# Kernel optimization log

Hardware: AMD Instinct MI355X
Metric: run time of the kernel (lower is better)

The kernel has to match this reference:

```python
import jax, jax.numpy as jnp
import numpy as np

NUM_HEADS = 16
D_MODEL = 1024


def setup_inputs() -> dict:
    key = jax.random.key(0)
    k1, k2 = jax.random.split(key)
    x = jax.random.normal(k1, (4, 2048, D_MODEL), dtype=jnp.float32)
    # kqv Linear(d_model, 3*d_model, bias=False); stored as [in, out] for x @ W
    W_kqv = jax.random.normal(k2, (D_MODEL, 3 * D_MODEL), dtype=jnp.float32) * (D_MODEL ** -0.5)
    return {"x": x, "W_kqv": W_kqv}


def _alibi_slopes(num_heads):
    # 1 / ((2**8)**((i+1)/num_heads)) for each head
    base = (2.0 ** 8) ** (1.0 / num_heads)
    return jnp.asarray([1.0 / base ** (i + 1) for i in range(num_heads)], dtype=jnp.float32)


def reference(x, W_kqv):
    B, S, D = x.shape
    H = NUM_HEADS
    hd = D // H
    scale = jnp.sqrt(jnp.float32(D))  # note: sqrt(d_model), faithful to source

    kqv = x @ W_kqv  # [B, S, 3D]; chunk order in source: key, query, value
    k, q, v = jnp.split(kqv, 3, axis=-1)
    # [B, H, S, hd]
    q = q.reshape(B, S, H, hd).transpose(0, 2, 1, 3)
    k = k.reshape(B, S, H, hd).transpose(0, 2, 1, 3)
    v = v.reshape(B, S, H, hd).transpose(0, 2, 1, 3)

    # ALiBi bias: m[h] * (j - i), shape [1, H, S, S]
    pos = jnp.arange(S)
    rel = (pos[None, :] - pos[:, None]).astype(jnp.float32)  # [S, S]
    m = _alibi_slopes(H)  # [H]
    bias = m[:, None, None] * rel  # [H, S, S]

    score = jnp.einsum('bhsd,bhnd->bhsn', q, k) / scale + bias[None]
    attn = jax.nn.softmax(score, axis=-1)
    out = jnp.einsum('bhsn,bhnd->bhsd', attn, v)  # [B, H, S, hd]
    out = out.transpose(0, 2, 1, 3).reshape(B, S, D)
    return out
```

## Files before the change

kernel.cpp:

```cpp
#include <hip/hip_runtime.h>
#include <stdint.h>

typedef __bf16 bf16;
typedef __bf16 bf16x4 __attribute__((ext_vector_type(4)));
typedef __bf16 bf16x8 __attribute__((ext_vector_type(8)));
typedef float f32x4 __attribute__((ext_vector_type(4)));

#define AS1 __attribute__((address_space(1)))
#define AS3 __attribute__((address_space(3)))


__global__ void cvt_x_kernel(const float* __restrict__ x, bf16* __restrict__ xb) {
    int i = blockIdx.x * 256 + threadIdx.x;
    const float4* x4 = (const float4*)x;
    float4 a = x4[i * 2];
    float4 b = x4[i * 2 + 1];
    bf16x8 o;
    o[0] = (bf16)a.x; o[1] = (bf16)a.y; o[2] = (bf16)a.z; o[3] = (bf16)a.w;
    o[4] = (bf16)b.x; o[5] = (bf16)b.y; o[6] = (bf16)b.z; o[7] = (bf16)b.w;
    *(bf16x8*)(xb + (size_t)i * 8) = o;
}

__global__ void cvt_w_kernel(const float* __restrict__ w, bf16* __restrict__ wt) {
    __shared__ float tile[32][33];
    int nt = blockIdx.x, kt = blockIdx.y;
    int tx = threadIdx.x, ty = threadIdx.y;
#pragma unroll
    for (int j = 0; j < 4; ++j)
        tile[ty + j * 8][tx] = w[(size_t)(kt * 32 + ty + j * 8) * 3072 + nt * 32 + tx];
    __syncthreads();
#pragma unroll
    for (int j = 0; j < 4; ++j)
        wt[(size_t)(nt * 32 + ty + j * 8) * 1024 + kt * 32 + tx] = (bf16)tile[tx][ty + j * 8];
}

__global__ __launch_bounds__(256) void gemm_kqv_kernel(
    const bf16* __restrict__ xb, const bf16* __restrict__ wt,
    bf16* __restrict__ kb, bf16* __restrict__ qb, bf16* __restrict__ vt) {
    __shared__ bf16 As[2][128 * 32];
    __shared__ bf16 Bs[2][128 * 32];
    int bid = blockIdx.x;
    int bm = bid / 24, bn = bid % 24;
    int m0 = bm * 128, n0 = bn * 128;
    int t = threadIdx.x;
    int lane = t & 63, wid = t >> 6;
    int g = lane >> 4, l15 = lane & 15;
    int wr = wid >> 1, wc = wid & 1;

    f32x4 acc[4][4] = {};

    auto stageAB = [&](int ks, int buf) {
        int k0 = ks * 32;
#pragma unroll
        for (int c = 0; c < 2; ++c) {
            int slot = c * 256 + t;
            int row = slot >> 2, kk = (slot & 3) * 8;
            __builtin_amdgcn_global_load_lds(
                (const AS1 void*)(xb + (size_t)(m0 + row) * 1024 + k0 + kk),
                (AS3 void*)(&As[buf][slot * 8]), 16, 0, 0);
        }
#pragma unroll
        for (int c = 0; c < 2; ++c) {
            int slot = c * 256 + t;
            int row = slot >> 2, kk = (slot & 3) * 8;
            __builtin_amdgcn_global_load_lds(
                (const AS1 void*)(wt + (size_t)(n0 + row) * 1024 + k0 + kk),
                (AS3 void*)(&Bs[buf][slot * 8]), 16, 0, 0);
        }
    };

    stageAB(0, 0);
    for (int ks = 0; ks < 32; ++ks) {
        __syncthreads();
        if (ks + 1 < 32) stageAB(ks + 1, (ks + 1) & 1);
        const bf16* Ab = As[ks & 1];
        const bf16* Bb = Bs[ks & 1];
        bf16x8 af[4], bfr[4];
#pragma unroll
        for (int mi = 0; mi < 4; ++mi)
            af[mi] = *(const bf16x8*)(Ab + (wr * 64 + mi * 16 + l15) * 32 + g * 8);
#pragma unroll
        for (int ni = 0; ni < 4; ++ni)
            bfr[ni] = *(const bf16x8*)(Bb + (wc * 64 + ni * 16 + l15) * 32 + g * 8);
#pragma unroll
        for (int mi = 0; mi < 4; ++mi)
#pragma unroll
            for (int ni = 0; ni < 4; ++ni)
                acc[mi][ni] = __builtin_amdgcn_mfma_f32_16x16x32_bf16(
                    af[mi], bfr[ni], acc[mi][ni], 0, 0, 0);
    }

    int tsel = n0 >> 10;
#pragma unroll
    for (int mi = 0; mi < 4; ++mi) {
#pragma unroll
        for (int ni = 0; ni < 4; ++ni) {
#pragma unroll
            for (int r = 0; r < 4; ++r) {
                int row = m0 + wr * 64 + mi * 16 + g * 4 + r;
                int col = n0 + wc * 64 + ni * 16 + l15;
                int b = row >> 11, s = row & 2047;
                int cc = col & 1023;
                int h = cc >> 6, d = cc & 63;
                int bh = b * 16 + h;
                float v = acc[mi][ni][r];
                if (tsel == 0)      kb[((size_t)bh * 2048 + s) * 64 + d] = (bf16)v;
                else if (tsel == 1) qb[((size_t)bh * 2048 + s) * 64 + d] = (bf16)(v * 0.0450842503f);
                else                vt[((size_t)bh * 64 + d) * 2048 + s] = (bf16)v;
            }
        }
    }
}

__global__ __launch_bounds__(256) void attn_kernel(
    const bf16* __restrict__ qb, const bf16* __restrict__ kb,
    const bf16* __restrict__ vt, float* __restrict__ out) {
    __shared__ bf16 Kl[64 * 64];
    __shared__ bf16 Vl[2][64 * 64];
    __shared__ bf16 Pl[4][32 * 64];
    int bid = blockIdx.x;
    int bh = bid >> 4, qt = bid & 15;
    int b = bh >> 4, h = bh & 15;
    int t = threadIdx.x, lane = t & 63, wid = t >> 6;
    int g = lane >> 4, l15 = lane & 15;
    int q0 = qt * 128 + wid * 32;
    float mh2 = exp2f(-0.5f * (float)(h + 1)) * 1.44269504f;

    const bf16* Qp = qb + ((size_t)bh * 2048 + q0) * 64;
    const bf16* Kp = kb + (size_t)bh * 2048 * 64;
    const bf16* Vp = vt + (size_t)bh * 64 * 2048;

    bf16x8 qf[2][2];
#pragma unroll
    for (int qi = 0; qi < 2; ++qi)
#pragma unroll
        for (int kk = 0; kk < 2; ++kk)
            qf[qi][kk] = *(const bf16x8*)(Qp + (size_t)(qi * 16 + l15) * 64 + kk * 32 + g * 8);

    f32x4 oacc[2][4] = {};
    float mrun[2], lrun[2];
    mrun[0] = mrun[1] = -3.0e38f;
    lrun[0] = lrun[1] = 0.f;

    float jb[4], rb[4];
#pragma unroll
    for (int ji = 0; ji < 4; ++ji) jb[ji] = mh2 * (float)(ji * 16 + g * 4);
#pragma unroll
    for (int r = 0; r < 4; ++r) rb[r] = mh2 * (float)r;

    auto stageK = [&](int tile) {
        int j0 = tile * 64;
#pragma unroll
        for (int c = 0; c < 2; ++c) {
            int slot = c * 256 + t;
            int row = slot >> 3;
            int cs = (slot & 7) ^ (row & 7);
            __builtin_amdgcn_global_load_lds(
                (const AS1 void*)(Kp + (size_t)(j0 + row) * 64 + cs * 8),
                (AS3 void*)(&Kl[slot * 8]), 16, 0, 0);
        }
    };
    auto stageV = [&](int tile, int buf) {
        int j0 = tile * 64;
#pragma unroll
        for (int c = 0; c < 2; ++c) {
            int slot = c * 256 + t;
            int row = slot >> 3;
            int cs = (slot & 7) ^ (row & 7);
            __builtin_amdgcn_global_load_lds(
                (const AS1 void*)(Vp + (size_t)row * 2048 + j0 + cs * 8),
                (AS3 void*)(&Vl[buf][slot * 8]), 16, 0, 0);
        }
    };

    stageK(0);
    stageV(0, 0);
    bf16* Pw = Pl[wid];

    for (int tile = 0; tile < 32; ++tile) {
        __syncthreads();
        const bf16* Vb = Vl[tile & 1];

        float tb = mh2 * (float)(tile * 64);
        f32x4 sc[2][4];
#pragma unroll
        for (int ji = 0; ji < 4; ++ji) {
            float base = tb + jb[ji];
#pragma unroll
            for (int r = 0; r < 4; ++r) {
                float v = base + rb[r];
                sc[0][ji][r] = v;
                sc[1][ji][r] = v;
            }
        }
#pragma unroll
        for (int ji = 0; ji < 4; ++ji) {
#pragma unroll
            for (int kk = 0; kk < 2; ++kk) {
                int row = ji * 16 + l15;
                int c16 = (kk * 4 + g) ^ (row & 7);
                bf16x8 kf = *(const bf16x8*)(Kl + row * 64 + c16 * 8);
#pragma unroll
                for (int qi = 0; qi < 2; ++qi)
                    sc[qi][ji] = __builtin_amdgcn_mfma_f32_16x16x32_bf16(
                        kf, qf[qi][kk], sc[qi][ji], 0, 0, 0);
            }
        }
        __syncthreads();
        if (tile + 1 < 32) {
            stageK(tile + 1);
            stageV(tile + 1, (tile + 1) & 1);
        }

        float pmx[2];
#pragma unroll
        for (int qi = 0; qi < 2; ++qi) {
            float m0a = fmaxf(fmaxf(sc[qi][0][0], sc[qi][0][1]), fmaxf(sc[qi][0][2], sc[qi][0][3]));
            float m1a = fmaxf(fmaxf(sc[qi][1][0], sc[qi][1][1]), fmaxf(sc[qi][1][2], sc[qi][1][3]));
            float m2a = fmaxf(fmaxf(sc[qi][2][0], sc[qi][2][1]), fmaxf(sc[qi][2][2], sc[qi][2][3]));
            float m3a = fmaxf(fmaxf(sc[qi][3][0], sc[qi][3][1]), fmaxf(sc[qi][3][2], sc[qi][3][3]));
            pmx[qi] = fmaxf(fmaxf(m0a, m1a), fmaxf(m2a, m3a));
        }

        int stable = (pmx[0] <= mrun[0] + 8.0f && pmx[1] <= mrun[1] + 8.0f) ? 1 : 0;
        if (!__all(stable)) {
            float corr[2];
#pragma unroll
            for (int qi = 0; qi < 2; ++qi) {
                float mx = pmx[qi];
                mx = fmaxf(mx, __shfl_xor(mx, 16));
                mx = fmaxf(mx, __shfl_xor(mx, 32));
                float mnew = fmaxf(mrun[qi], mx);
                corr[qi] = __builtin_amdgcn_exp2f(mrun[qi] - mnew);
                mrun[qi] = mnew;
                lrun[qi] *= corr[qi];
            }
#pragma unroll
            for (int qi = 0; qi < 2; ++qi)
#pragma unroll
                for (int r = 0; r < 4; ++r) {
                    float cB = __shfl(corr[qi], g * 4 + r);
#pragma unroll
                    for (int di = 0; di < 4; ++di) oacc[qi][di][r] *= cB;
                }
        }

#pragma unroll
        for (int qi = 0; qi < 2; ++qi) {
            float mq = mrun[qi];
            float s = 0.f;
#pragma unroll
            for (int ji = 0; ji < 4; ++ji)
#pragma unroll
                for (int r = 0; r < 4; ++r) {
                    float p = __builtin_amdgcn_exp2f(sc[qi][ji][r] - mq);
                    sc[qi][ji][r] = p;
                    s += p;
                }
            s += __shfl_xor(s, 16);
            s += __shfl_xor(s, 32);
            lrun[qi] += s;
        }

#pragma unroll
        for (int qi = 0; qi < 2; ++qi) {
            int qloc = qi * 16 + l15;
            int base = qloc * 64;
            int swz = (qloc & 7) * 8;
#pragma unroll
            for (int ji = 0; ji < 4; ++ji) {
                bf16x4 pv;
                pv[0] = (bf16)sc[qi][ji][0];
                pv[1] = (bf16)sc[qi][ji][1];
                pv[2] = (bf16)sc[qi][ji][2];
                pv[3] = (bf16)sc[qi][ji][3];
                *(bf16x4*)(Pw + base + ((ji * 16 + g * 4) ^ swz)) = pv;
            }
        }

#pragma unroll
        for (int kk = 0; kk < 2; ++kk) {
            bf16x8 pf[2];
#pragma unroll
            for (int qi = 0; qi < 2; ++qi) {
                int qloc = qi * 16 + l15;
                pf[qi] = *(const bf16x8*)(Pw + qloc * 64 + ((kk * 32 + g * 8) ^ ((qloc & 7) * 8)));
            }
#pragma unroll
            for (int di = 0; di < 4; ++di) {
                int row = di * 16 + l15;
                int c16 = (kk * 4 + g) ^ (row & 7);
                bf16x8 vf = *(const bf16x8*)(Vb + row * 64 + c16 * 8);
#pragma unroll
                for (int qi = 0; qi < 2; ++qi)
                    oacc[qi][di] = __builtin_amdgcn_mfma_f32_16x16x32_bf16(
                        pf[qi], vf, oacc[qi][di], 0, 0, 0);
            }
        }
    }

#pragma unroll
    for (int qi = 0; qi < 2; ++qi) {
#pragma unroll
        for (int r = 0; r < 4; ++r) {
            float lq = __shfl(lrun[qi], g * 4 + r);
            float inv = 1.0f / lq;
            int s = q0 + qi * 16 + g * 4 + r;
            float* op = out + ((size_t)b * 2048 + s) * 1024 + h * 64;
#pragma unroll
            for (int di = 0; di < 4; ++di)
                op[di * 16 + l15] = oacc[qi][di][r] * inv;
        }
    }
}

extern "C" void kernel_launch(void* const* d_in, const int* in_sizes, int n_in,
                              void* d_out, int out_size, void* d_ws, size_t ws_size,
                              hipStream_t stream) {
    (void)in_sizes; (void)n_in; (void)out_size; (void)ws_size;
    const float* x = (const float*)d_in[0];
    const float* w = (const float*)d_in[1];
    float* out = (float*)d_out;
    char* ws = (char*)d_ws;
    bf16* xb = (bf16*)(ws);
    bf16* wt = (bf16*)(ws + 16777216);
    bf16* kb = (bf16*)(ws + 23068672);
    bf16* qb = (bf16*)(ws + 39845888);
    bf16* vt = (bf16*)(ws + 56623104);

    cvt_x_kernel<<<4096, 256, 0, stream>>>(x, xb);
    cvt_w_kernel<<<dim3(96, 32), dim3(32, 8), 0, stream>>>(w, wt);
    gemm_kqv_kernel<<<1536, 256, 0, stream>>>(xb, wt, kb, qb, vt);
    attn_kernel<<<1024, 256, 0, stream>>>(qb, kb, vt, out);
}
```

Measured before the change: 311.7 us.

## Fold running max into score init, use 3-input max, vectorize V-transpose stores

The attention kernel now subtracts the running max when it seeds the MFMA accumulator with the ALiBi bias. This removes the per-element subtraction before exp2 in the common path, and the max reduction is regrouped into three-input fmax calls. The initial running max changes from -3e38 to -10000 to avoid overflow in the folded form, which assumes scores never fall that low. The QKV projection epilogue is restructured with hoisted index math and bf16x4 vector stores for the transposed V output.

```diff
diff --git a/kernel.cpp b/kernel.cpp
--- a/kernel.cpp
+++ b/kernel.cpp
@@ -9,6 +9,10 @@
 #define AS1 __attribute__((address_space(1)))
 #define AS3 __attribute__((address_space(3)))
 
+
+__device__ __forceinline__ float f3(float a, float b, float c) {
+    return fmaxf(fmaxf(a, b), c);
+}
 
 __global__ void cvt_x_kernel(const float* __restrict__ x, bf16* __restrict__ xb) {
     int i = blockIdx.x * 256 + threadIdx.x;
@@ -91,24 +95,39 @@
     }
 
     int tsel = n0 >> 10;
-#pragma unroll
-    for (int mi = 0; mi < 4; ++mi) {
+    int hbase = (n0 >> 6) & 15;
+    int bidx = m0 >> 11;
+    int m0b = (m0 & 2047) + wr * 64 + g * 4;
+    int bh = bidx * 16 + hbase + wc;
+    if (tsel == 2) {
 #pragma unroll
         for (int ni = 0; ni < 4; ++ni) {
-#pragma unroll
-            for (int r = 0; r < 4; ++r) {
-                int row = m0 + wr * 64 + mi * 16 + g * 4 + r;
-                int col = n0 + wc * 64 + ni * 16 + l15;
-                int b = row >> 11, s = row & 2047;
-                int cc = col & 1023;
-                int h = cc >> 6, d = cc & 63;
-                int bh = b * 16 + h;
-                float v = acc[mi][ni][r];
-                if (tsel == 0)      kb[((size_t)bh * 2048 + s) * 64 + d] = (bf16)v;
-                else if (tsel == 1) qb[((size_t)bh * 2048 + s) * 64 + d] = (bf16)(v * 0.0450842503f);
-                else                vt[((size_t)bh * 64 + d) * 2048 + s] = (bf16)v;
-            }
-        }
+            int d = ni * 16 + l15;
+            bf16* vbase = vt + ((size_t)bh * 64 + d) * 2048 + m0b;
+#pragma unroll
+            for (int mi = 0; mi < 4; ++mi) {
+                bf16x4 pv;
+                pv[0] = (bf16)acc[mi][ni][0];
+                pv[1] = (bf16)acc[mi][ni][1];
+                pv[2] = (bf16)acc[mi][ni][2];
+                pv[3] = (bf16)acc[mi][ni][3];
+                *(bf16x4*)(vbase + mi * 16) = pv;
+            }
+        }
+    } else {
+        bf16* dst = (tsel == 0) ? kb : qb;
+        float sc = (tsel == 0) ? 1.0f : 0.0450842503f;
+#pragma unroll
+        for (int mi = 0; mi < 4; ++mi)
+#pragma unroll
+            for (int ni = 0; ni < 4; ++ni) {
+                int d = ni * 16 + l15;
+#pragma unroll
+                for (int r = 0; r < 4; ++r) {
+                    int s = m0b + mi * 16 + r;
+                    dst[((size_t)bh * 2048 + s) * 64 + d] = (bf16)(acc[mi][ni][r] * sc);
+                }
+            }
     }
 }
 
@@ -139,7 +158,7 @@
 
     f32x4 oacc[2][4] = {};
     float mrun[2], lrun[2];
-    mrun[0] = mrun[1] = -3.0e38f;
+    mrun[0] = mrun[1] = -10000.0f;
     lrun[0] = lrun[1] = 0.f;
 
     float jb[4], rb[4];
@@ -184,13 +203,13 @@
         float tb = mh2 * (float)(tile * 64);
         f32x4 sc[2][4];
 #pragma unroll
-        for (int ji = 0; ji < 4; ++ji) {
-            float base = tb + jb[ji];
-#pragma unroll
-            for (int r = 0; r < 4; ++r) {
-                float v = base + rb[r];
-                sc[0][ji][r] = v;
-                sc[1][ji][r] = v;
+        for (int qi = 0; qi < 2; ++qi) {
+            float bq = tb - mrun[qi];
+#pragma unroll
+            for (int ji = 0; ji < 4; ++ji) {
+                float base = bq + jb[ji];
+#pragma unroll
+                for (int r = 0; r < 4; ++r) sc[qi][ji][r] = base + rb[r];
             }
         }
 #pragma unroll
@@ -215,26 +234,35 @@
         float pmx[2];
 #pragma unroll
         for (int qi = 0; qi < 2; ++qi) {
-            float m0a = fmaxf(fmaxf(sc[qi][0][0], sc[qi][0][1]), fmaxf(sc[qi][0][2], sc[qi][0][3]));
-            float m1a = fmaxf(fmaxf(sc[qi][1][0], sc[qi][1][1]), fmaxf(sc[qi][1][2], sc[qi][1][3]));
-            float m2a = fmaxf(fmaxf(sc[qi][2][0], sc[qi][2][1]), fmaxf(sc[qi][2][2], sc[qi][2][3]));
-            float m3a = fmaxf(fmaxf(sc[qi][3][0], sc[qi][3][1]), fmaxf(sc[qi][3][2], sc[qi][3][3]));
-            pmx[qi] = fmaxf(fmaxf(m0a, m1a), fmaxf(m2a, m3a));
-        }
-
-        int stable = (pmx[0] <= mrun[0] + 8.0f && pmx[1] <= mrun[1] + 8.0f) ? 1 : 0;
+            float a0 = f3(sc[qi][0][0], sc[qi][0][1], sc[qi][0][2]);
+            float a1 = f3(sc[qi][0][3], sc[qi][1][0], sc[qi][1][1]);
+            float a2 = f3(sc[qi][1][2], sc[qi][1][3], sc[qi][2][0]);
+            float a3 = f3(sc[qi][2][1], sc[qi][2][2], sc[qi][2][3]);
+            float a4 = f3(sc[qi][3][0], sc[qi][3][1], sc[qi][3][2]);
+            float a5 = fmaxf(sc[qi][3][3], f3(a0, a1, a2));
+            pmx[qi] = f3(a3, a4, a5);
+        }
+
+        int stable = (pmx[0] <= 8.0f && pmx[1] <= 8.0f) ? 1 : 0;
         if (!__all(stable)) {
-            float corr[2];
+            float dm[2], corr[2];
 #pragma unroll
             for (int qi = 0; qi < 2; ++qi) {
                 float mx = pmx[qi];
                 mx = fmaxf(mx, __shfl_xor(mx, 16));
                 mx = fmaxf(mx, __shfl_xor(mx, 32));
-                float mnew = fmaxf(mrun[qi], mx);
-                corr[qi] = __builtin_amdgcn_exp2f(mrun[qi] - mnew);
-                mrun[qi] = mnew;
+                float d = fmaxf(mx, 0.0f);
+                dm[qi] = d;
+                corr[qi] = __builtin_amdgcn_exp2f(-d);
+                mrun[qi] += d;
                 lrun[qi] *= corr[qi];
             }
+#pragma unroll
+            for (int qi = 0; qi < 2; ++qi)
+#pragma unroll
+                for (int ji = 0; ji < 4; ++ji)
+#pragma unroll
+                    for (int r = 0; r < 4; ++r) sc[qi][ji][r] -= dm[qi];
 #pragma unroll
             for (int qi = 0; qi < 2; ++qi)
 #pragma unroll
@@ -247,13 +275,12 @@
 
 #pragma unroll
         for (int qi = 0; qi < 2; ++qi) {
-            float mq = mrun[qi];
             float s = 0.f;
 #pragma unroll
             for (int ji = 0; ji < 4; ++ji)
 #pragma unroll
                 for (int r = 0; r < 4; ++r) {
-                    float p = __builtin_amdgcn_exp2f(sc[qi][ji][r] - mq);
+                    float p = __builtin_amdgcn_exp2f(sc[qi][ji][r]);
                     sc[qi][ji][r] = p;
                     s += p;
                 }
```

Result: faster. 304.2 us (-2.4%).
